# Performance work log

Hardware: AMD Instinct MI355X
Metric: run time of the kernel (lower is better)

Reference implementation:

```python
import jax, jax.numpy as jnp
from jax import lax
import numpy as np

B, T, D_IN, H, OUT = 64, 512, 512, 1024, 128


def setup_inputs() -> dict:
    key = jax.random.key(0)
    ks = jax.random.split(key, 12)
    s = 0.02
    return {
        "x": jax.random.normal(ks[0], (B, T, D_IN), dtype=jnp.float32),
        "W_ih0": jax.random.normal(ks[1], (H, D_IN), dtype=jnp.float32) * s,
        "W_hh0": jax.random.normal(ks[2], (H, H), dtype=jnp.float32) * s,
        "b_ih0": jax.random.normal(ks[3], (H,), dtype=jnp.float32) * s,
        "b_hh0": jax.random.normal(ks[4], (H,), dtype=jnp.float32) * s,
        "W_ih1": jax.random.normal(ks[5], (H, H), dtype=jnp.float32) * s,
        "W_hh1": jax.random.normal(ks[6], (H, H), dtype=jnp.float32) * s,
        "b_ih1": jax.random.normal(ks[7], (H,), dtype=jnp.float32) * s,
        "b_hh1": jax.random.normal(ks[8], (H,), dtype=jnp.float32) * s,
        "W_fc": jax.random.normal(ks[9], (OUT, H), dtype=jnp.float32) * s,
        "b_fc": jax.random.normal(ks[10], (OUT,), dtype=jnp.float32) * s,
    }


def _rnn_layer(seq, W_ih, W_hh, b_ih, b_hh):
    # seq: [B, T, D] -> outputs [B, T, H]; h_t = tanh(x_t W_ih^T + b_ih + h_{t-1} W_hh^T + b_hh)
    pre = jnp.einsum("btd,hd->bth", seq, W_ih) + b_ih + b_hh  # one big input GEMM
    h0 = jnp.zeros((seq.shape[0], W_hh.shape[0]), dtype=seq.dtype)

    def step(h, p_t):
        h_new = jnp.tanh(p_t + h @ W_hh.T)
        return h_new, h_new

    _, hs = lax.scan(step, h0, jnp.swapaxes(pre, 0, 1))  # [T, B, H]
    return jnp.swapaxes(hs, 0, 1)  # [B, T, H]


def reference(x, W_ih0, W_hh0, b_ih0, b_hh0, W_ih1, W_hh1, b_ih1, b_hh1, W_fc, b_fc):
    h1 = _rnn_layer(x, W_ih0, W_hh0, b_ih0, b_hh0)
    h2 = _rnn_layer(h1, W_ih1, W_hh1, b_ih1, b_hh1)
    last = h2[:, -1, :]  # [B, H]
    return last @ W_fc.T + b_fc  # [B, OUT]
```

## Files before the change

### kernel.cpp

```cpp
#include <hip/hip_runtime.h>
#include <stdint.h>
#include <stddef.h>

#define Bn   64
#define Tn   512
#define DINn 512
#define Hn   1024
#define OUTn 128

typedef __attribute__((ext_vector_type(4))) float f32x4;
typedef __attribute__((ext_vector_type(8))) short short8;
typedef __attribute__((ext_vector_type(4))) unsigned int u32x4;

__device__ __forceinline__ unsigned short f2bf(float f){
  unsigned int x = __builtin_bit_cast(unsigned int, f);
  x += 0x7fffu + ((x >> 16) & 1u);
  return (unsigned short)(x >> 16);
}
__device__ __forceinline__ float bf2f(unsigned short u){
  return __builtin_bit_cast(float, (unsigned int)u << 16);
}
__device__ __forceinline__ float tanh_fast(float v){
  float e = __expf(2.0f * v);
  return 1.0f - 2.0f / (e + 1.0f);
}

template<bool FAST>
__device__ __forceinline__ void st16(unsigned short* p, u32x4 v){
  if constexpr (FAST)
    asm volatile("global_store_dwordx4 %0, %1, off sc0" :: "v"(p), "v"(v) : "memory");
  else
    asm volatile("global_store_dwordx4 %0, %1, off sc0 sc1" :: "v"(p), "v"(v) : "memory");
}
__device__ __forceinline__ unsigned atom_poll(unsigned int* p){
  unsigned old, zero = 0;
  asm volatile("global_atomic_add %0, %1, %2, off sc0\n\t"
               "s_waitcnt vmcnt(0)"
               : "=&v"(old) : "v"(p), "v"(zero) : "memory");
  return old;
}
__device__ __forceinline__ void atom_poll2(unsigned int* p1, unsigned int* p2,
                                           unsigned &v1, unsigned &v2){
  unsigned zero = 0;
  asm volatile("global_atomic_add %0, %2, %4, off sc0\n\t"
               "global_atomic_add %1, %3, %4, off sc0\n\t"
               "s_waitcnt vmcnt(0)"
               : "=&v"(v1), "=&v"(v2)
               : "v"(p1), "v"(p2), "v"(zero) : "memory");
}
__device__ __forceinline__ void atom_inc(unsigned int* p){
  unsigned one = 1;
  asm volatile("global_atomic_add %0, %1, off" :: "v"(p), "v"(one) : "memory");
}
__device__ __forceinline__ unsigned ld1_sc0(const unsigned int* p){
  unsigned v;
  asm volatile("global_load_dword %0, %1, off sc0\n\t"
               "s_waitcnt vmcnt(0)" : "=&v"(v) : "v"(p) : "memory");
  return v;
}
__device__ __forceinline__ unsigned umin4(u32x4 a){
  unsigned m0 = a[0] < a[1] ? a[0] : a[1];
  unsigned m1 = a[2] < a[3] ? a[2] : a[3];
  return m0 < m1 ? m0 : m1;
}
__device__ __forceinline__ unsigned ld_line8_slow(const unsigned int* p){
  u32x4 a, b;
  asm volatile("global_load_dwordx4 %0, %2, off sc0 sc1\n\t"
               "global_load_dwordx4 %1, %3, off sc0 sc1\n\t"
               "s_waitcnt vmcnt(0)"
               : "=&v"(a), "=&v"(b) : "v"(p), "v"(p + 4) : "memory");
  unsigned ma = umin4(a), mb = umin4(b);
  return ma < mb ? ma : mb;
}
template<bool FAST>
__device__ __forceinline__ void wait_one(unsigned int* fc, unsigned int* fl, unsigned wf8, unsigned wslow){
  if constexpr (FAST){
    if (!wf8) return;
    for (int i = 0; i < (1 << 16); ++i){
      if (atom_poll(fc) >= wf8) return;
      __builtin_amdgcn_s_sleep(2);
    }
  } else {
    if (!wslow) return;
    for (int i = 0; i < (1 << 16); ++i){
      if (ld_line8_slow(fl) >= wslow) return;
      if (i > 16) __builtin_amdgcn_s_sleep(1);
    }
  }
}
template<bool FAST>
__device__ __forceinline__ void wait_dual(unsigned int* fc1, unsigned int* fl1, unsigned wf1, unsigned ws1,
                                          unsigned int* fc2, unsigned int* fl2, unsigned wf2, unsigned ws2){
  if constexpr (FAST){
    if (!wf2){ wait_one<true>(fc1, fl1, wf1, ws1); return; }
    for (int i = 0; i < (1 << 16); ++i){
      unsigned v1, v2;
      atom_poll2(fc1, fc2, v1, v2);
      if (v1 >= wf1 && v2 >= wf2) return;
      __builtin_amdgcn_s_sleep(2);
    }
  } else {
    if (!ws2){ wait_one<false>(fc1, fl1, wf1, ws1); return; }
    for (int i = 0; i < (1 << 16); ++i){
      if (ld_line8_slow(fl1) >= ws1 && ld_line8_slow(fl2) >= ws2) return;
      if (i > 16) __builtin_amdgcn_s_sleep(1);
    }
  }
}

template<bool FAST>
__device__ __forceinline__ void stage_lin(const unsigned short* base, unsigned short* hl, int tid){
  const unsigned short* p0 = base + (size_t)tid * 8;
  const unsigned short* p1 = p0 + 512 * 8;
  u32x4 v0, v1;
  if constexpr (FAST)
    asm volatile("global_load_dwordx4 %0, %2, off sc0\n\t"
                 "global_load_dwordx4 %1, %3, off sc0\n\t"
                 "s_waitcnt vmcnt(0)"
                 : "=&v"(v0), "=&v"(v1) : "v"(p0), "v"(p1) : "memory");
  else
    asm volatile("global_load_dwordx4 %0, %2, off sc0 sc1\n\t"
                 "global_load_dwordx4 %1, %3, off sc0 sc1\n\t"
                 "s_waitcnt vmcnt(0)"
                 : "=&v"(v0), "=&v"(v1) : "v"(p0), "v"(p1) : "memory");
  *(u32x4*)((char*)hl + tid * 16) = v0;
  *(u32x4*)((char*)hl + tid * 16 + 8192) = v1;
}
template<bool FAST>
__device__ __forceinline__ void ld4_chunk(const unsigned short* p, float* pv){
  unsigned u0,u1,u2,u3;
  if constexpr (FAST)
    asm volatile("global_load_ushort %0, %4, off sc0\n\t"
                 "global_load_ushort %1, %5, off sc0\n\t"
                 "global_load_ushort %2, %6, off sc0\n\t"
                 "global_load_ushort %3, %7, off sc0\n\t"
                 "s_waitcnt vmcnt(0)"
                 : "=&v"(u0), "=&v"(u1), "=&v"(u2), "=&v"(u3)
                 : "v"(p), "v"(p + 8), "v"(p + 16), "v"(p + 24) : "memory");
  else
    asm volatile("global_load_ushort %0, %4, off sc0 sc1\n\t"
                 "global_load_ushort %1, %5, off sc0 sc1\n\t"
                 "global_load_ushort %2, %6, off sc0 sc1\n\t"
                 "global_load_ushort %3, %7, off sc0 sc1\n\t"
                 "s_waitcnt vmcnt(0)"
                 : "=&v"(u0), "=&v"(u1), "=&v"(u2), "=&v"(u3)
                 : "v"(p), "v"(p + 8), "v"(p + 16), "v"(p + 24) : "memory");
  pv[0] = bf2f((unsigned short)u0); pv[1] = bf2f((unsigned short)u1);
  pv[2] = bf2f((unsigned short)u2); pv[3] = bf2f((unsigned short)u3);
}

__device__ __forceinline__ f32x4 mfma_tile(const char* lbase, const short8* wf, int lrow, int kh){
  f32x4 a0 = {0.f,0.f,0.f,0.f}, a1 = a0, a2 = a0, a3 = a0;
  int rb = kh * 128 + lrow * 16;
#pragma unroll
  for (int kk = 0; kk < 8; ++kk)
    a0 = __builtin_amdgcn_mfma_f32_16x16x32_bf16(*(const short8*)(lbase + kk*512 + rb), wf[kk], a0, 0,0,0);
#pragma unroll
  for (int kk = 8; kk < 16; ++kk)
    a1 = __builtin_amdgcn_mfma_f32_16x16x32_bf16(*(const short8*)(lbase + kk*512 + rb), wf[kk], a1, 0,0,0);
#pragma unroll
  for (int kk = 16; kk < 24; ++kk)
    a2 = __builtin_amdgcn_mfma_f32_16x16x32_bf16(*(const short8*)(lbase + kk*512 + rb), wf[kk], a2, 0,0,0);
#pragma unroll
  for (int kk = 24; kk < 32; ++kk)
    a3 = __builtin_amdgcn_mfma_f32_16x16x32_bf16(*(const short8*)(lbase + kk*512 + rb), wf[kk], a3, 0,0,0);
  return (a0 + a1) + (a2 + a3);
}

__global__ void cvt_bf16x8(const float* __restrict__ in, unsigned short* __restrict__ out,
                           long long n8){
  long long i = (long long)blockIdx.x * blockDim.x + threadIdx.x;
  long long stride = (long long)gridDim.x * blockDim.x;
  for (; i < n8; i += stride){
    const float* p = in + i*8;
    float4 a = *(const float4*)p;
    float4 b = *(const float4*)(p+4);
    short8 v;
    v[0]=(short)f2bf(a.x); v[1]=(short)f2bf(a.y); v[2]=(short)f2bf(a.z); v[3]=(short)f2bf(a.w);
    v[4]=(short)f2bf(b.x); v[5]=(short)f2bf(b.y); v[6]=(short)f2bf(b.z); v[7]=(short)f2bf(b.w);
    *(short8*)(out + i*8) = v;
  }
}

__global__ void bias_combine(const float* __restrict__ a, const float* __restrict__ b, float* __restrict__ o,
                             const float* __restrict__ c, const float* __restrict__ d, float* __restrict__ p){
  int i = blockIdx.x * blockDim.x + threadIdx.x;
  if (i < Hn){ o[i] = a[i] + b[i]; p[i] = c[i] + d[i]; }
}

__launch_bounds__(256, 2)
__global__ void gemm_pre0(const float* __restrict__ Av, const unsigned short* __restrict__ Bm,
                          const float* __restrict__ bias, unsigned short* __restrict__ C,
                          int N, int K)
{
  __shared__ unsigned short lA[128*64];
  __shared__ unsigned short lB[128*64];
  int bn = blockIdx.x, bm = blockIdx.y;
  int m0 = bm*128, n0 = bn*128;
  int tid = threadIdx.x, lane = tid & 63, w = tid >> 6;
  int wm = (w >> 1)*64, wn = (w & 1)*64;
  int cl = lane & 15, kh = lane >> 4;

  f32x4 acc[4][4];
  f32x4 z = {0.f,0.f,0.f,0.f};
#pragma unroll
  for (int i=0;i<4;i++)
#pragma unroll
    for (int j=0;j<4;j++) acc[i][j]=z;

  for (int k0 = 0; k0 < K; k0 += 64){
    __syncthreads();
#pragma unroll
    for (int r = 0; r < 4; ++r){
      int c = r*256 + tid;
      int row = c >> 3, cof = (c & 7)*8;
      const float* ap = Av + (size_t)(m0+row)*K + k0 + cof;
      float4 a = *(const float4*)ap;
      float4 b = *(const float4*)(ap+4);
      short8 v;
      v[0]=(short)f2bf(a.x); v[1]=(short)f2bf(a.y); v[2]=(short)f2bf(a.z); v[3]=(short)f2bf(a.w);
      v[4]=(short)f2bf(b.x); v[5]=(short)f2bf(b.y); v[6]=(short)f2bf(b.z); v[7]=(short)f2bf(b.w);
      *(short8*)&lA[row*64 + cof] = v;
      const unsigned short* bp = Bm + (size_t)(n0+row)*K + k0 + cof;
      *(short8*)&lB[row*64 + cof] = *(const short8*)bp;
    }
    __syncthreads();
#pragma unroll
    for (int kk = 0; kk < 2; ++kk){
      int kb = kk*32 + kh*8;
      short8 af[4], bfr[4];
#pragma unroll
      for (int i=0;i<4;i++) af[i]  = *(const short8*)&lA[(wm + i*16 + cl)*64 + kb];
#pragma unroll
      for (int j=0;j<4;j++) bfr[j] = *(const short8*)&lB[(wn + j*16 + cl)*64 + kb];
#pragma unroll
      for (int i=0;i<4;i++)
#pragma unroll
        for (int j=0;j<4;j++)
          acc[i][j] = __builtin_amdgcn_mfma_f32_16x16x32_bf16(af[i], bfr[j], acc[i][j], 0,0,0);
    }
  }
#pragma unroll
  for (int j=0;j<4;j++){
    int n = n0 + wn + j*16 + cl;
    float bs = bias[n];
#pragma unroll
    for (int i=0;i<4;i++){
      int mr = m0 + wm + i*16 + kh*4;
#pragma unroll
      for (int e=0;e<4;e++){
        int m = mr + e;
        int b = m >> 9, t = m & (Tn-1);
        C[((size_t)t*Bn + b)*N + n] = f2bf(acc[i][j][e] + bs);
      }
    }
  }
}

template<bool FAST>
__device__ __forceinline__ void rnn_body(
    int role, int g, int slot, int tid, int w, int lane, int cl, int kh, int lrow,
    const unsigned short* pre0, unsigned short* bufP, unsigned short* h1buf,
    const float* bias1,
    unsigned int* FCA0, unsigned int* FCA1, unsigned int* FCB, unsigned int* FCC,
    unsigned int* FLA, unsigned int* FLB, unsigned int* FLC,
    const short8* wf, unsigned short* hl, unsigned short* outl)
{
  const char* lbase = (const char*)hl;
  int n0 = slot*128 + w*16;
  int olocal = w*128 + ((cl>>3)*8 + kh*4)*8 + (cl&7);
  unsigned int* myFL = ((role == 0) ? FLA : (role == 1) ? FLB : FLC) + slot;

  for (int t = 0; t < Tn; ++t){
    float pv[4] = {0.f,0.f,0.f,0.f};
    if (role == 0 && kh < 2){
      const unsigned short* pp = pre0 + ((size_t)t*Bn + g*8 + kh*4)*Hn + n0 + cl;
#pragma unroll
      for (int j=0;j<4;j++) pv[j] = bf2f(pp[(size_t)j*Hn]);
    }
    if (tid == 0){
      if (role == 0)      wait_one <FAST>(FCA0, FLA, 8u*(unsigned)t, (unsigned)t);
      else if (role == 1) wait_one <FAST>(FCA1, FLA, 8u*(unsigned)(t+1), (unsigned)(t+1));
      else                wait_dual<FAST>(FCB, FLB, 8u*(unsigned)(t+1), (unsigned)(t+1),
                                          FCC, FLC, 8u*(unsigned)t, (unsigned)t);
    }
    __syncthreads();
    bool staged = true;
    if (role == 0){
      if (t > 0) stage_lin<FAST>(h1buf + ((size_t)(t+1)*8 + g)*8192, hl, tid);
      else staged = false;
    } else if (role == 1){
      stage_lin<FAST>(h1buf + ((size_t)(t+2)*8 + g)*8192, hl, tid);
    } else {
      if (kh < 2)
        ld4_chunk<FAST>(h1buf + ((size_t)t*8 + g)*8192 + slot*1024 + ((w*16+cl)>>3)*64 + kh*32 + (cl&7), pv);
      if (t > 0) stage_lin<FAST>(bufP + ((size_t)(t-1)*Bn + g*8)*Hn, hl, tid);
      else staged = false;
    }
    __syncthreads();
    f32x4 acc = {0.f,0.f,0.f,0.f};
    if (staged) acc = mfma_tile(lbase, wf, lrow, kh);
    if (kh < 2){
      float bs = (role == 1) ? bias1[n0 + cl] : 0.f;
#pragma unroll
      for (int j=0;j<4;j++){
        float v = acc[j] + pv[j] + bs;
        if (role != 1) v = tanh_fast(v);
        outl[olocal + j*8] = f2bf(v);
      }
    }
    unsigned short* tile;
    if (role == 0)      tile = h1buf + ((size_t)(t+2)*8 + g)*8192;
    else if (role == 1) tile = h1buf + ((size_t)t*8 + g)*8192;
    else                tile = bufP + ((size_t)t*Bn + g*8)*Hn;
    if (lane < 16){
      u32x4 v = *(const u32x4*)(outl + w*128 + lane*8);
      st16<FAST>(tile + slot*1024 + (w*16 + lane)*8, v);
    }
    asm volatile("s_waitcnt vmcnt(0)" ::: "memory");
    __syncthreads();
    if (tid == 0){
      if constexpr (FAST){
        if (role == 0){ atom_inc(FCA0); atom_inc(FCA1); }
        else if (role == 1) atom_inc(FCB);
        else atom_inc(FCC);
      } else {
        asm volatile("global_store_dword %0, %1, off sc0 sc1" :: "v"(myFL), "v"((unsigned)(t+1)) : "memory");
      }
    }
  }
}

__launch_bounds__(512, 2)
__global__ void rnn_fused(const unsigned short* __restrict__ pre0_ro,
                          unsigned short* __restrict__ bufP,
                          unsigned short* __restrict__ h1buf,
                          const float* __restrict__ Whh0,
                          const float* __restrict__ Wih1,
                          const float* __restrict__ Whh1,
                          const float* __restrict__ bias1,
                          unsigned int* ctrs)
{
  __shared__ __align__(16) unsigned short hl[8192];
  __shared__ __align__(16) unsigned short outl[1024];
  __shared__ int s_fast;
  int bx = blockIdx.x;
  int g = bx & 7;
  int sub = bx >> 3;
  int role = sub >> 3, slot = sub & 7;
  int tid = threadIdx.x, lane = tid & 63, w = tid >> 6;
  int n0 = slot*128 + w*16;
  int cl = lane & 15, kh = lane >> 4, lrow = cl & 7;
  unsigned int* FLA = ctrs + (0*8 + g)*32;
  unsigned int* FLB = ctrs + (1*8 + g)*32;
  unsigned int* FLC = ctrs + (2*8 + g)*32;
  unsigned int* arrive1 = ctrs + 768;
  unsigned int* badf    = ctrs + 772;
  unsigned int* arrive2 = ctrs + 776;
  unsigned int* FCA0 = ctrs + 1536 + (0*8 + g)*32;
  unsigned int* FCB  = ctrs + 1536 + (1*8 + g)*32;
  unsigned int* FCC  = ctrs + 1536 + (2*8 + g)*32;
  unsigned int* FCA1 = ctrs + 1536 + (3*8 + g)*32;

  if (tid == 0){
    int xcc;
    asm volatile("s_getreg_b32 %0, hwreg(HW_REG_XCC_ID)" : "=s"(xcc));
    unsigned int* testw = ctrs + 1024 + g*32;
    unsigned int* armed = testw + 16;
    if (xcc != g)
      __hip_atomic_fetch_or(badf, 1u, __ATOMIC_RELAXED, __HIP_MEMORY_SCOPE_AGENT);
    __hip_atomic_fetch_add(arrive1, 1u, __ATOMIC_ACQ_REL, __HIP_MEMORY_SCOPE_AGENT);
    int t1 = 0;
    for (int i = 0; i < (1 << 20); ++i){
      if (__hip_atomic_load(arrive1, __ATOMIC_ACQUIRE, __HIP_MEMORY_SCOPE_AGENT) >= 192u){ t1 = 1; break; }
      __builtin_amdgcn_s_sleep(2);
    }
    if (!t1) __hip_atomic_fetch_or(badf, 1u, __ATOMIC_RELAXED, __HIP_MEMORY_SCOPE_AGENT);
    unsigned magic = 0xC0FFEE00u | (unsigned)g;
    if (sub == 0){
      asm volatile("global_store_dword %0, %1, off sc0\n\t"
                   "s_waitcnt vmcnt(0)" :: "v"(testw), "v"(magic) : "memory");
      atom_inc(armed);
    }
    int ok = 0;
    for (int i = 0; i < (1 << 15); ++i){
      if (atom_poll(armed) >= 1u){ ok = (ld1_sc0(testw) == magic); break; }
      if (i > 16) __builtin_amdgcn_s_sleep(1);
    }
    if (!ok) __hip_atomic_fetch_or(badf, 1u, __ATOMIC_RELAXED, __HIP_MEMORY_SCOPE_AGENT);
    __hip_atomic_fetch_add(arrive2, 1u, __ATOMIC_ACQ_REL, __HIP_MEMORY_SCOPE_AGENT);
    int t2 = 0;
    for (int i = 0; i < (1 << 20); ++i){
      if (__hip_atomic_load(arrive2, __ATOMIC_ACQUIRE, __HIP_MEMORY_SCOPE_AGENT) >= 192u){ t2 = 1; break; }
      __builtin_amdgcn_s_sleep(2);
    }
    unsigned bad = __hip_atomic_load(badf, __ATOMIC_ACQUIRE, __HIP_MEMORY_SCOPE_AGENT);
    s_fast = (t2 && bad == 0u) ? 1 : 0;
  }
  __syncthreads();
  const bool fast = (s_fast != 0);

  const float* Wmat = (role == 0) ? Whh0 : (role == 1) ? Wih1 : Whh1;
  short8 wf[32];
  {
    const float* wr = Wmat + (size_t)(n0 + cl)*Hn + kh*8;
#pragma unroll
    for (int kk = 0; kk < 32; ++kk){
      float4 a = *(const float4*)(wr + kk*32);
      float4 b = *(const float4*)(wr + kk*32 + 4);
      short8 v;
      v[0]=(short)f2bf(a.x); v[1]=(short)f2bf(a.y); v[2]=(short)f2bf(a.z); v[3]=(short)f2bf(a.w);
      v[4]=(short)f2bf(b.x); v[5]=(short)f2bf(b.y); v[6]=(short)f2bf(b.z); v[7]=(short)f2bf(b.w);
      wf[kk] = v;
    }
  }

  if (fast)
    rnn_body<true >(role, g, slot, tid, w, lane, cl, kh, lrow, pre0_ro, bufP, h1buf,
                    bias1, FCA0, FCA1, FCB, FCC, FLA, FLB, FLC, wf, hl, outl);
  else
    rnn_body<false>(role, g, slot, tid, w, lane, cl, kh, lrow, pre0_ro, bufP, h1buf,
                    bias1, FCA0, FCA1, FCB, FCC, FLA, FLB, FLC, wf, hl, outl);
}

__global__ void fc_k(const unsigned short* __restrict__ bufP,
                     const float* __restrict__ Wfc, const float* __restrict__ bfc,
                     float* __restrict__ out)
{
  int gw = (blockIdx.x * blockDim.x + threadIdx.x) >> 6;
  int lane = threadIdx.x & 63;
  int b = gw >> 7, o = gw & 127;
  const unsigned short* tile = bufP + ((size_t)(Tn-1)*Bn + (b & ~7))*Hn;
  int r = b & 7;
  const float* wr = Wfc + (size_t)o*Hn;
  float s = 0.f;
  for (int k = lane; k < Hn; k += 64)
    s += bf2f(tile[((k>>3)*8 + r)*8 + (k&7)]) * wr[k];
#pragma unroll
  for (int off = 32; off > 0; off >>= 1) s += __shfl_down(s, off, 64);
  if (lane == 0) out[b*OUTn + o] = s + bfc[o];
}

extern "C" void kernel_launch(void* const* d_in, const int* in_sizes, int n_in,
                              void* d_out, int out_size, void* d_ws, size_t ws_size,
                              hipStream_t stream)
{
  const float* x    = (const float*)d_in[0];
  const float* Wih0 = (const float*)d_in[1];
  const float* Whh0 = (const float*)d_in[2];
  const float* bih0 = (const float*)d_in[3];
  const float* bhh0 = (const float*)d_in[4];
  const float* Wih1 = (const float*)d_in[5];
  const float* Whh1 = (const float*)d_in[6];
  const float* bih1 = (const float*)d_in[7];
  const float* bhh1 = (const float*)d_in[8];
  const float* Wfc  = (const float*)d_in[9];
  const float* bfc  = (const float*)d_in[10];
  float* out = (float*)d_out;

  unsigned short* bufP  = (unsigned short*)d_ws;
  unsigned short* h1buf = bufP  + (size_t)Bn*Tn*Hn;
  unsigned short* wih0b = h1buf + (size_t)(Tn+2)*8*8192;
  float* bias0 = (float*)(wih0b + (size_t)Hn*DINn);
  float* bias1 = bias0 + Hn;
  unsigned int* ctrs = (unsigned int*)(bias1 + Hn);

  hipMemsetAsync(ctrs, 0, 4096*sizeof(unsigned int), stream);

  cvt_bf16x8<<<256, 256, 0, stream>>>(Wih0, wih0b, (long long)Hn*DINn/8);
  bias_combine<<<4, 256, 0, stream>>>(bih0, bhh0, bias0, bih1, bhh1, bias1);

  dim3 g1(Hn/128, (Bn*Tn)/128);
  gemm_pre0<<<g1, 256, 0, stream>>>(x, wih0b, bias0, bufP, Hn, DINn);

  rnn_fused<<<192, 512, 0, stream>>>(bufP, bufP, h1buf, Whh0, Wih1, Whh1, bias1, ctrs);

  fc_k<<<2048, 256, 0, stream>>>(bufP, Wfc, bfc, out);
}
```

Before: 1.384 ms.

## Add nontemporal per-slot flag polling mode for inter-block step synchronisation

Adds a third synchronisation mode in which each producer block stores its step count to its own flag slot with a plain store, and consumers poll eight flags at once using nontemporal loads, instead of polling atomic counters. A runtime self-test at startup checks whether nontemporal loads see cross-CU stores, and chooses between the new mode, the old atomic mode and the slow coherent fallback. The spin-wait sleep is also shortened and now starts only after a few polls. The aim is to cut per-timestep handshake latency in the persistent RNN loop. The cost is an extra startup test phase and reliance on hardware cache behaviour for correctness.

```diff
diff --git a/kernel.cpp b/kernel.cpp
--- a/kernel.cpp
+++ b/kernel.cpp
@@ -58,6 +58,12 @@
                "s_waitcnt vmcnt(0)" : "=&v"(v) : "v"(p) : "memory");
   return v;
 }
+__device__ __forceinline__ unsigned ld1_nt(const unsigned int* p){
+  unsigned v;
+  asm volatile("global_load_dword %0, %1, off nt\n\t"
+               "s_waitcnt vmcnt(0)" : "=&v"(v) : "v"(p) : "memory");
+  return v;
+}
 __device__ __forceinline__ unsigned umin4(u32x4 a){
   unsigned m0 = a[0] < a[1] ? a[0] : a[1];
   unsigned m1 = a[2] < a[3] ? a[2] : a[3];
@@ -72,13 +78,47 @@
   unsigned ma = umin4(a), mb = umin4(b);
   return ma < mb ? ma : mb;
 }
+__device__ __forceinline__ unsigned ld_line8_nt(const unsigned int* p){
+  u32x4 a, b;
+  asm volatile("global_load_dwordx4 %0, %2, off nt\n\t"
+               "global_load_dwordx4 %1, %3, off nt\n\t"
+               "s_waitcnt vmcnt(0)"
+               : "=&v"(a), "=&v"(b) : "v"(p), "v"(p + 4) : "memory");
+  unsigned ma = umin4(a), mb = umin4(b);
+  return ma < mb ? ma : mb;
+}
+__device__ __forceinline__ void wait8_nt(const unsigned int* p, unsigned want){
+  if (!want) return;
+  for (int i = 0; i < (1 << 16); ++i){
+    if (ld_line8_nt(p) >= want) return;
+    if (i > 8) __builtin_amdgcn_s_sleep(1);
+  }
+}
+__device__ __forceinline__ void wait8_nt2(const unsigned int* p1, unsigned w1,
+                                          const unsigned int* p2, unsigned w2){
+  if (!w2){ wait8_nt(p1, w1); return; }
+  for (int i = 0; i < (1 << 16); ++i){
+    u32x4 a, b, c, d;
+    asm volatile("global_load_dwordx4 %0, %4, off nt\n\t"
+                 "global_load_dwordx4 %1, %5, off nt\n\t"
+                 "global_load_dwordx4 %2, %6, off nt\n\t"
+                 "global_load_dwordx4 %3, %7, off nt\n\t"
+                 "s_waitcnt vmcnt(0)"
+                 : "=&v"(a), "=&v"(b), "=&v"(c), "=&v"(d)
+                 : "v"(p1), "v"(p1 + 4), "v"(p2), "v"(p2 + 4) : "memory");
+    unsigned m1 = umin4(a) < umin4(b) ? umin4(a) : umin4(b);
+    unsigned m2 = umin4(c) < umin4(d) ? umin4(c) : umin4(d);
+    if (m1 >= w1 && m2 >= w2) return;
+    if (i > 8) __builtin_amdgcn_s_sleep(1);
+  }
+}
 template<bool FAST>
-__device__ __forceinline__ void wait_one(unsigned int* fc, unsigned int* fl, unsigned wf8, unsigned wslow){
+__device__ __forceinline__ void wait_one(unsigned int* fc, unsigned int* fl, unsigned wfast, unsigned wslow){
   if constexpr (FAST){
-    if (!wf8) return;
+    if (!wfast) return;
     for (int i = 0; i < (1 << 16); ++i){
-      if (atom_poll(fc) >= wf8) return;
-      __builtin_amdgcn_s_sleep(2);
+      if (atom_poll(fc) >= wfast) return;
+      if (i > 8) __builtin_amdgcn_s_sleep(1);
     }
   } else {
     if (!wslow) return;
@@ -97,7 +137,7 @@
       unsigned v1, v2;
       atom_poll2(fc1, fc2, v1, v2);
       if (v1 >= wf1 && v2 >= wf2) return;
-      __builtin_amdgcn_s_sleep(2);
+      if (i > 8) __builtin_amdgcn_s_sleep(1);
     }
   } else {
     if (!ws2){ wait_one<false>(fc1, fl1, wf1, ws1); return; }
@@ -111,7 +151,7 @@
 template<bool FAST>
 __device__ __forceinline__ void stage_lin(const unsigned short* base, unsigned short* hl, int tid){
   const unsigned short* p0 = base + (size_t)tid * 8;
-  const unsigned short* p1 = p0 + 512 * 8;
+  const unsigned short* p1 = p0 + 4096;
   u32x4 v0, v1;
   if constexpr (FAST)
     asm volatile("global_load_dwordx4 %0, %2, off sc0\n\t"
@@ -257,19 +297,22 @@
   }
 }
 
-template<bool FAST>
+template<int MODE>
 __device__ __forceinline__ void rnn_body(
     int role, int g, int slot, int tid, int w, int lane, int cl, int kh, int lrow,
     const unsigned short* pre0, unsigned short* bufP, unsigned short* h1buf,
     const float* bias1,
     unsigned int* FCA0, unsigned int* FCA1, unsigned int* FCB, unsigned int* FCC,
     unsigned int* FLA, unsigned int* FLB, unsigned int* FLC,
+    unsigned int* FNA, unsigned int* FNB, unsigned int* FNC,
     const short8* wf, unsigned short* hl, unsigned short* outl)
 {
+  constexpr bool FAST = (MODE < 2);
   const char* lbase = (const char*)hl;
   int n0 = slot*128 + w*16;
   int olocal = w*128 + ((cl>>3)*8 + kh*4)*8 + (cl&7);
   unsigned int* myFL = ((role == 0) ? FLA : (role == 1) ? FLB : FLC) + slot;
+  unsigned int* myFN = ((role == 0) ? FNA : (role == 1) ? FNB : FNC) + slot;
 
   for (int t = 0; t < Tn; ++t){
     float pv[4] = {0.f,0.f,0.f,0.f};
@@ -279,10 +322,16 @@
       for (int j=0;j<4;j++) pv[j] = bf2f(pp[(size_t)j*Hn]);
     }
     if (tid == 0){
-      if (role == 0)      wait_one <FAST>(FCA0, FLA, 8u*(unsigned)t, (unsigned)t);
-      else if (role == 1) wait_one <FAST>(FCA1, FLA, 8u*(unsigned)(t+1), (unsigned)(t+1));
-      else                wait_dual<FAST>(FCB, FLB, 8u*(unsigned)(t+1), (unsigned)(t+1),
-                                          FCC, FLC, 8u*(unsigned)t, (unsigned)t);
+      if constexpr (MODE == 0){
+        if (role == 0)      wait8_nt(FNA, (unsigned)t);
+        else if (role == 1) wait8_nt(FNA, (unsigned)(t+1));
+        else                wait8_nt2(FNB, (unsigned)(t+1), FNC, (unsigned)t);
+      } else {
+        if (role == 0)      wait_one <FAST>(FCA0, FLA, 8u*(unsigned)t, (unsigned)t);
+        else if (role == 1) wait_one <FAST>(FCA1, FLA, 8u*(unsigned)(t+1), (unsigned)(t+1));
+        else                wait_dual<FAST>(FCB, FLB, 8u*(unsigned)(t+1), (unsigned)(t+1),
+                                            FCC, FLC, 8u*(unsigned)t, (unsigned)t);
+      }
     }
     __syncthreads();
     bool staged = true;
@@ -320,7 +369,9 @@
     asm volatile("s_waitcnt vmcnt(0)" ::: "memory");
     __syncthreads();
     if (tid == 0){
-      if constexpr (FAST){
+      if constexpr (MODE == 0){
+        asm volatile("global_store_dword %0, %1, off sc0" :: "v"(myFN), "v"((unsigned)(t+1)) : "memory");
+      } else if constexpr (MODE == 1){
         if (role == 0){ atom_inc(FCA0); atom_inc(FCA1); }
         else if (role == 1) atom_inc(FCB);
         else atom_inc(FCC);
@@ -343,7 +394,7 @@
 {
   __shared__ __align__(16) unsigned short hl[8192];
   __shared__ __align__(16) unsigned short outl[1024];
-  __shared__ int s_fast;
+  __shared__ int s_mode;
   int bx = blockIdx.x;
   int g = bx & 7;
   int sub = bx >> 3;
@@ -355,50 +406,86 @@
   unsigned int* FLB = ctrs + (1*8 + g)*32;
   unsigned int* FLC = ctrs + (2*8 + g)*32;
   unsigned int* arrive1 = ctrs + 768;
-  unsigned int* badf    = ctrs + 772;
+  unsigned int* badAT   = ctrs + 772;
   unsigned int* arrive2 = ctrs + 776;
+  unsigned int* badNT   = ctrs + 780;
+  unsigned int* arrive3 = ctrs + 784;
   unsigned int* FCA0 = ctrs + 1536 + (0*8 + g)*32;
   unsigned int* FCB  = ctrs + 1536 + (1*8 + g)*32;
   unsigned int* FCC  = ctrs + 1536 + (2*8 + g)*32;
   unsigned int* FCA1 = ctrs + 1536 + (3*8 + g)*32;
+  unsigned int* FNA = ctrs + 2560 + (0*8 + g)*32;
+  unsigned int* FNB = ctrs + 2560 + (1*8 + g)*32;
+  unsigned int* FNC = ctrs + 2560 + (2*8 + g)*32;
 
   if (tid == 0){
     int xcc;
     asm volatile("s_getreg_b32 %0, hwreg(HW_REG_XCC_ID)" : "=s"(xcc));
-    unsigned int* testw = ctrs + 1024 + g*32;
-    unsigned int* armed = testw + 16;
-    if (xcc != g)
-      __hip_atomic_fetch_or(badf, 1u, __ATOMIC_RELAXED, __HIP_MEMORY_SCOPE_AGENT);
+    unsigned int* atw = ctrs + 1024 + g*32;  unsigned int* atarmed = atw + 16;
+    unsigned int* ntw = ctrs + 3328 + g*32;  unsigned int* ntarmed = ntw + 16;
+    if (xcc != g){
+      __hip_atomic_fetch_or(badNT, 1u, __ATOMIC_RELAXED, __HIP_MEMORY_SCOPE_AGENT);
+      __hip_atomic_fetch_or(badAT, 1u, __ATOMIC_RELAXED, __HIP_MEMORY_SCOPE_AGENT);
+    }
+    unsigned pr = ld1_nt(ntw) + ld1_nt(ntarmed);
+    asm volatile("" :: "v"(pr));
     __hip_atomic_fetch_add(arrive1, 1u, __ATOMIC_ACQ_REL, __HIP_MEMORY_SCOPE_AGENT);
     int t1 = 0;
     for (int i = 0; i < (1 << 20); ++i){
       if (__hip_atomic_load(arrive1, __ATOMIC_ACQUIRE, __HIP_MEMORY_SCOPE_AGENT) >= 192u){ t1 = 1; break; }
       __builtin_amdgcn_s_sleep(2);
     }
-    if (!t1) __hip_atomic_fetch_or(badf, 1u, __ATOMIC_RELAXED, __HIP_MEMORY_SCOPE_AGENT);
-    unsigned magic = 0xC0FFEE00u | (unsigned)g;
+    if (!t1){
+      __hip_atomic_fetch_or(badNT, 1u, __ATOMIC_RELAXED, __HIP_MEMORY_SCOPE_AGENT);
+      __hip_atomic_fetch_or(badAT, 1u, __ATOMIC_RELAXED, __HIP_MEMORY_SCOPE_AGENT);
+    }
+    unsigned magicN = 0xBEEF0000u | (unsigned)g;
     if (sub == 0){
       asm volatile("global_store_dword %0, %1, off sc0\n\t"
-                   "s_waitcnt vmcnt(0)" :: "v"(testw), "v"(magic) : "memory");
-      atom_inc(armed);
-    }
-    int ok = 0;
-    for (int i = 0; i < (1 << 15); ++i){
-      if (atom_poll(armed) >= 1u){ ok = (ld1_sc0(testw) == magic); break; }
-      if (i > 16) __builtin_amdgcn_s_sleep(1);
-    }
-    if (!ok) __hip_atomic_fetch_or(badf, 1u, __ATOMIC_RELAXED, __HIP_MEMORY_SCOPE_AGENT);
+                   "s_waitcnt vmcnt(0)\n\t"
+                   "global_store_dword %2, %3, off sc0"
+                   :: "v"(ntw), "v"(magicN), "v"(ntarmed), "v"(1u) : "memory");
+    }
+    int okN = 0;
+    for (int i = 0; i < (1 << 14); ++i){
+      if (ld1_nt(ntarmed) == 1u){ okN = (ld1_nt(ntw) == magicN); break; }
+      if (i > 8) __builtin_amdgcn_s_sleep(1);
+    }
+    if (!okN) __hip_atomic_fetch_or(badNT, 1u, __ATOMIC_RELAXED, __HIP_MEMORY_SCOPE_AGENT);
     __hip_atomic_fetch_add(arrive2, 1u, __ATOMIC_ACQ_REL, __HIP_MEMORY_SCOPE_AGENT);
     int t2 = 0;
     for (int i = 0; i < (1 << 20); ++i){
       if (__hip_atomic_load(arrive2, __ATOMIC_ACQUIRE, __HIP_MEMORY_SCOPE_AGENT) >= 192u){ t2 = 1; break; }
       __builtin_amdgcn_s_sleep(2);
     }
-    unsigned bad = __hip_atomic_load(badf, __ATOMIC_ACQUIRE, __HIP_MEMORY_SCOPE_AGENT);
-    s_fast = (t2 && bad == 0u) ? 1 : 0;
+    if (!t2){
+      __hip_atomic_fetch_or(badNT, 1u, __ATOMIC_RELAXED, __HIP_MEMORY_SCOPE_AGENT);
+      __hip_atomic_fetch_or(badAT, 1u, __ATOMIC_RELAXED, __HIP_MEMORY_SCOPE_AGENT);
+    }
+    unsigned magicA = 0xCAFE0000u | (unsigned)g;
+    if (sub == 0){
+      asm volatile("global_store_dword %0, %1, off sc0\n\t"
+                   "s_waitcnt vmcnt(0)" :: "v"(atw), "v"(magicA) : "memory");
+      atom_inc(atarmed);
+    }
+    int okA = 0;
+    for (int i = 0; i < (1 << 15); ++i){
+      if (atom_poll(atarmed) >= 1u){ okA = (ld1_sc0(atw) == magicA); break; }
+      if (i > 16) __builtin_amdgcn_s_sleep(1);
+    }
+    if (!okA) __hip_atomic_fetch_or(badAT, 1u, __ATOMIC_RELAXED, __HIP_MEMORY_SCOPE_AGENT);
+    __hip_atomic_fetch_add(arrive3, 1u, __ATOMIC_ACQ_REL, __HIP_MEMORY_SCOPE_AGENT);
+    int t3 = 0;
+    for (int i = 0; i < (1 << 20); ++i){
+      if (__hip_atomic_load(arrive3, __ATOMIC_ACQUIRE, __HIP_MEMORY_SCOPE_AGENT) >= 192u){ t3 = 1; break; }
+      __builtin_amdgcn_s_sleep(2);
+    }
+    unsigned bN = __hip_atomic_load(badNT, __ATOMIC_ACQUIRE, __HIP_MEMORY_SCOPE_AGENT);
+    unsigned bA = __hip_atomic_load(badAT, __ATOMIC_ACQUIRE, __HIP_MEMORY_SCOPE_AGENT);
+    s_mode = (!t3) ? 2 : (bN == 0u ? 0 : (bA == 0u ? 1 : 2));
   }
   __syncthreads();
-  const bool fast = (s_fast != 0);
+  const int mode = s_mode;
 
   const float* Wmat = (role == 0) ? Whh0 : (role == 1) ? Wih1 : Whh1;
   short8 wf[32];
@@ -415,12 +502,15 @@
     }
   }
 
-  if (fast)
-    rnn_body<true >(role, g, slot, tid, w, lane, cl, kh, lrow, pre0_ro, bufP, h1buf,
-                    bias1, FCA0, FCA1, FCB, FCC, FLA, FLB, FLC, wf, hl, outl);
+  if (mode == 0)
+    rnn_body<0>(role, g, slot, tid, w, lane, cl, kh, lrow, pre0_ro, bufP, h1buf,
+                bias1, FCA0, FCA1, FCB, FCC, FLA, FLB, FLC, FNA, FNB, FNC, wf, hl, outl);
+  else if (mode == 1)
+    rnn_body<1>(role, g, slot, tid, w, lane, cl, kh, lrow, pre0_ro, bufP, h1buf,
+                bias1, FCA0, FCA1, FCB, FCC, FLA, FLB, FLC, FNA, FNB, FNC, wf, hl, outl);
   else
-    rnn_body<false>(role, g, slot, tid, w, lane, cl, kh, lrow, pre0_ro, bufP, h1buf,
-                    bias1, FCA0, FCA1, FCB, FCC, FLA, FLB, FLC, wf, hl, outl);
+    rnn_body<2>(role, g, slot, tid, w, lane, cl, kh, lrow, pre0_ro, bufP, h1buf,
+                bias1, FCA0, FCA1, FCB, FCC, FLA, FLB, FLC, FNA, FNB, FNC, wf, hl, outl);
 }
 
 __global__ void fc_k(const unsigned short* __restrict__ bufP,
```

Result: faster. 1.199 ms (-13.3%).
